# Kernel tuning notes

Measured on AMD Instinct MI355X. Metric: run time of the kernel, lower is better.

## Reference

```python
import jax, jax.numpy as jnp
import numpy as np

N, D, T = 4096, 512, 4096
TEMPERATURE = 0.07
MARGIN = 0.5
CONT_WEIGHT = 1.0
TRIP_WEIGHT = 0.3
EPS = 1e-8        # eps in the log / denominator (matches torch code)
PD_EPS = 1e-6     # F.pairwise_distance default eps added to the difference


def setup_inputs() -> dict:
    key = jax.random.key(0)
    k1, k2, k3 = jax.random.split(key, 3)
    embeddings = jax.random.normal(k1, (N, D), dtype=jnp.float32)
    labels = jax.random.randint(k2, (N,), 0, 256)            # ~16 positives per place
    triplets = jax.random.randint(k3, (T, 3), 0, N)          # (anchor, pos, neg) indices
    return {"embeddings": embeddings, "labels": labels, "triplets": triplets}


def reference(embeddings, labels, triplets):
    # ---- MultiPositiveContrastiveLoss ----
    # F.cosine_similarity normalizes each row with eps=1e-8 on the norm.
    norms = jnp.linalg.norm(embeddings, axis=1, keepdims=True)
    n_emb = embeddings / jnp.maximum(norms, EPS)
    sim = (n_emb @ n_emb.T) / TEMPERATURE                    # [N, N]

    pos_mask = (labels[:, None] == labels[None, :]).astype(embeddings.dtype)
    pos_mask = pos_mask * (1.0 - jnp.eye(sim.shape[0], dtype=embeddings.dtype))

    exp_sim = jnp.exp(sim)
    pos_sum = (exp_sim * pos_mask).sum(axis=1)
    total_sum = exp_sim.sum(axis=1)
    loss = -jnp.log(pos_sum / (total_sum + EPS) + EPS)

    valid = pos_mask.sum(axis=1) > 0
    cnt = valid.sum()
    cont_loss = jnp.where(
        cnt > 0,
        jnp.where(valid, loss, 0.0).sum() / jnp.maximum(cnt, 1).astype(loss.dtype),
        jnp.zeros((), loss.dtype),
    )

    # ---- TripletLoss, vectorized over all triplets (replaces Python loop) ----
    a = embeddings[triplets[:, 0]]   # [T, D]
    p = embeddings[triplets[:, 1]]
    ng = embeddings[triplets[:, 2]]
    pos_dist = jnp.linalg.norm(a - p + PD_EPS, axis=1)
    neg_dist = jnp.linalg.norm(a - ng + PD_EPS, axis=1)
    trip_loss = jnp.maximum(pos_dist - neg_dist + MARGIN, 0.0).mean()

    total = CONT_WEIGHT * cont_loss + TRIP_WEIGHT * trip_loss
    return (total, cont_loss, trip_loss)
```

## Files before the change

### kernel.cpp

```cpp
#include <hip/hip_runtime.h>

#define NN 4096
#define DD 512
#define TT 4096

typedef __bf16 bf16x8 __attribute__((ext_vector_type(8)));
typedef float f32x4 __attribute__((ext_vector_type(4)));

constexpr float INV_TEMP = 1.0f / 0.07f;

#define AS1(p) ((__attribute__((address_space(1))) const void*)(p))
#define AS3(p) ((__attribute__((address_space(3))) void*)(p))

__global__ __launch_bounds__(256) void k_normalize(const float* __restrict__ emb,
                                                   __bf16* __restrict__ nemb) {
    int wave = threadIdx.x >> 6, lane = threadIdx.x & 63;
    int row = blockIdx.x * 4 + wave;
    const float4* src = (const float4*)(emb + (size_t)row * DD);
    float4 x0 = src[lane * 2 + 0];
    float4 x1 = src[lane * 2 + 1];
    float ss = x0.x * x0.x + x0.y * x0.y + x0.z * x0.z + x0.w * x0.w +
               x1.x * x1.x + x1.y * x1.y + x1.z * x1.z + x1.w * x1.w;
    #pragma unroll
    for (int m = 1; m < 64; m <<= 1) ss += __shfl_xor(ss, m, 64);
    float inv = 1.0f / fmaxf(sqrtf(ss), 1e-8f);
    bf16x8 v;
    v[0] = (__bf16)(x0.x * inv); v[1] = (__bf16)(x0.y * inv);
    v[2] = (__bf16)(x0.z * inv); v[3] = (__bf16)(x0.w * inv);
    v[4] = (__bf16)(x1.x * inv); v[5] = (__bf16)(x1.y * inv);
    v[6] = (__bf16)(x1.z * inv); v[7] = (__bf16)(x1.w * inv);
    *(bf16x8*)(nemb + (size_t)row * DD + lane * 8) = v;
}

__global__ __launch_bounds__(256) void k_conttrip(const __bf16* __restrict__ nemb,
                                                  const int* __restrict__ labels,
                                                  const float* __restrict__ emb,
                                                  const int* __restrict__ trip,
                                                  float* __restrict__ posP,
                                                  float* __restrict__ totP,
                                                  float* __restrict__ cntP,
                                                  float* __restrict__ tl) {
    int tid = threadIdx.x;
    int lane = tid & 63, wave = tid >> 6;

    if (blockIdx.x >= 1024) {
        int t = (blockIdx.x - 1024) * 4 + wave;
        int ia = trip[t * 3 + 0], ip = trip[t * 3 + 1], ig = trip[t * 3 + 2];
        const float4* pa = (const float4*)(emb + (size_t)ia * DD);
        const float4* pp = (const float4*)(emb + (size_t)ip * DD);
        const float4* pn = (const float4*)(emb + (size_t)ig * DD);
        float d1 = 0.0f, d2 = 0.0f;
        #pragma unroll
        for (int j = 0; j < 2; ++j) {
            float4 a = pa[lane * 2 + j];
            float4 p = pp[lane * 2 + j];
            float4 n = pn[lane * 2 + j];
            float dx;
            dx = a.x - p.x + 1e-6f; d1 += dx * dx;
            dx = a.y - p.y + 1e-6f; d1 += dx * dx;
            dx = a.z - p.z + 1e-6f; d1 += dx * dx;
            dx = a.w - p.w + 1e-6f; d1 += dx * dx;
            dx = a.x - n.x + 1e-6f; d2 += dx * dx;
            dx = a.y - n.y + 1e-6f; d2 += dx * dx;
            dx = a.z - n.z + 1e-6f; d2 += dx * dx;
            dx = a.w - n.w + 1e-6f; d2 += dx * dx;
        }
        #pragma unroll
        for (int m = 1; m < 64; m <<= 1) {
            d1 += __shfl_xor(d1, m, 64);
            d2 += __shfl_xor(d2, m, 64);
        }
        if (lane == 0) tl[t] = fmaxf(sqrtf(d1) - sqrtf(d2) + 0.5f, 0.0f);
        return;
    }

    __shared__ __attribute__((aligned(16))) __bf16 aSm[128 * 64];
    __shared__ __attribute__((aligned(16))) __bf16 bSm[128 * 64];
    __shared__ int rlab[128];
    __shared__ int clab[128];

    int wr = wave >> 1, wc = wave & 1;
    int l15 = lane & 15, quad = lane >> 4;
    int rowblk = blockIdx.x >> 5, colblk = blockIdx.x & 31;
    int row0 = rowblk * 128, col0 = colblk * 128;

    if (tid < 128) rlab[tid] = labels[row0 + tid];
    else           clab[tid - 128] = labels[col0 + tid - 128];

    f32x4 acc[4][4];
    #pragma unroll
    for (int r = 0; r < 4; ++r)
        #pragma unroll
        for (int c = 0; c < 4; ++c) {
            f32x4 z = {0.0f, 0.0f, 0.0f, 0.0f};
            acc[r][c] = z;
        }

    const __bf16* gA = nemb + (size_t)(row0 + (tid >> 3)) * DD + (tid & 7) * 8;
    const __bf16* gB = nemb + (size_t)(col0 + (tid >> 3)) * DD + (tid & 7) * 8;

    for (int kt = 0; kt < 8; ++kt) {
        int kb = kt * 64;
        __syncthreads();
        #pragma unroll
        for (int op = 0; op < 4; ++op) {
            __builtin_amdgcn_global_load_lds(AS1(gA + (size_t)(32 * op) * DD + kb),
                                             AS3(aSm + op * 2048 + tid * 8), 16, 0, 0);
            __builtin_amdgcn_global_load_lds(AS1(gB + (size_t)(32 * op) * DD + kb),
                                             AS3(bSm + op * 2048 + tid * 8), 16, 0, 0);
        }
        __syncthreads();

        #pragma unroll
        for (int kc = 0; kc < 2; ++kc) {
            bf16x8 af[4], bfr[4];
            #pragma unroll
            for (int r = 0; r < 4; ++r)
                af[r] = *(const bf16x8*)(aSm + (wr * 64 + r * 16 + l15) * 64 + kc * 32 + quad * 8);
            #pragma unroll
            for (int c = 0; c < 4; ++c)
                bfr[c] = *(const bf16x8*)(bSm + (wc * 64 + c * 16 + l15) * 64 + kc * 32 + quad * 8);
            #pragma unroll
            for (int r = 0; r < 4; ++r)
                #pragma unroll
                for (int c = 0; c < 4; ++c)
                    acc[r][c] = __builtin_amdgcn_mfma_f32_16x16x32_bf16(af[r], bfr[c], acc[r][c], 0, 0, 0);
        }
    }

    int cl[4];
    #pragma unroll
    for (int c = 0; c < 4; ++c) cl[c] = clab[wc * 64 + c * 16 + l15];

    #pragma unroll
    for (int r = 0; r < 4; ++r) {
        float tv[4] = {0, 0, 0, 0}, pv[4] = {0, 0, 0, 0}, cv[4] = {0, 0, 0, 0};
        int gibase = row0 + wr * 64 + r * 16 + quad * 4;
        int rl[4];
        #pragma unroll
        for (int v = 0; v < 4; ++v) rl[v] = rlab[wr * 64 + r * 16 + quad * 4 + v];
        #pragma unroll
        for (int c = 0; c < 4; ++c) {
            int gj = col0 + wc * 64 + c * 16 + l15;
            #pragma unroll
            for (int v = 0; v < 4; ++v) {
                float e = __expf(acc[r][c][v] * INV_TEMP);
                tv[v] += e;
                bool match = (rl[v] == cl[c]) && ((gibase + v) != gj);
                pv[v] += match ? e : 0.0f;
                cv[v] += match ? 1.0f : 0.0f;
            }
        }
        #pragma unroll
        for (int m = 1; m < 16; m <<= 1) {
            #pragma unroll
            for (int v = 0; v < 4; ++v) {
                tv[v] += __shfl_xor(tv[v], m, 64);
                pv[v] += __shfl_xor(pv[v], m, 64);
                cv[v] += __shfl_xor(cv[v], m, 64);
            }
        }
        if (l15 == 0) {
            #pragma unroll
            for (int v = 0; v < 4; ++v) {
                int gr = gibase + v;
                int oidx = gr * 64 + colblk * 2 + wc;
                posP[oidx] = pv[v];
                totP[oidx] = tv[v];
                cntP[oidx] = cv[v];
            }
        }
    }
}

__global__ __launch_bounds__(256) void k_rowloss(const float* __restrict__ posP,
                                                 const float* __restrict__ totP,
                                                 const float* __restrict__ cntP,
                                                 float* __restrict__ rloss,
                                                 float* __restrict__ rvalid) {
    int wave = threadIdx.x >> 6, lane = threadIdx.x & 63;
    int row = blockIdx.x * 4 + wave;
    float p = posP[row * 64 + lane];
    float t = totP[row * 64 + lane];
    float c = cntP[row * 64 + lane];
    #pragma unroll
    for (int m = 1; m < 64; m <<= 1) {
        p += __shfl_xor(p, m, 64);
        t += __shfl_xor(t, m, 64);
        c += __shfl_xor(c, m, 64);
    }
    if (lane == 0) {
        float loss = -logf(p / (t + 1e-8f) + 1e-8f);
        bool valid = c > 0.0f;
        rloss[row] = valid ? loss : 0.0f;
        rvalid[row] = valid ? 1.0f : 0.0f;
    }
}

__global__ __launch_bounds__(256) void k_final(const float* __restrict__ rloss,
                                               const float* __restrict__ rvalid,
                                               const float* __restrict__ tl,
                                               float* __restrict__ out) {
    int tid = threadIdx.x;
    float sl = 0.0f, sv = 0.0f, st = 0.0f;
    for (int i = tid; i < NN; i += 256) {
        sl += rloss[i];
        sv += rvalid[i];
        st += tl[i];
    }
    #pragma unroll
    for (int m = 1; m < 64; m <<= 1) {
        sl += __shfl_xor(sl, m, 64);
        sv += __shfl_xor(sv, m, 64);
        st += __shfl_xor(st, m, 64);
    }
    __shared__ float red[3][4];
    int lane = tid & 63, wave = tid >> 6;
    if (lane == 0) { red[0][wave] = sl; red[1][wave] = sv; red[2][wave] = st; }
    __syncthreads();
    if (tid == 0) {
        float SL = red[0][0] + red[0][1] + red[0][2] + red[0][3];
        float SV = red[1][0] + red[1][1] + red[1][2] + red[1][3];
        float ST = red[2][0] + red[2][1] + red[2][2] + red[2][3];
        float cont = (SV > 0.0f) ? (SL / SV) : 0.0f;
        float trip = ST * (1.0f / (float)TT);
        out[0] = cont + 0.3f * trip;
        out[1] = cont;
        out[2] = trip;
    }
}

extern "C" void kernel_launch(void* const* d_in, const int* in_sizes, int n_in,
                              void* d_out, int out_size, void* d_ws, size_t ws_size,
                              hipStream_t stream) {
    const float* emb = (const float*)d_in[0];
    const int* labels = (const int*)d_in[1];
    const int* trips = (const int*)d_in[2];
    float* out = (float*)d_out;
    char* ws = (char*)d_ws;

    __bf16* nemb  = (__bf16*)(ws);
    float* posP   = (float*)(ws + 4194304);
    float* totP   = (float*)(ws + 5242880);
    float* cntP   = (float*)(ws + 6291456);
    float* rloss  = (float*)(ws + 7340032);
    float* rvalid = (float*)(ws + 7356416);
    float* tl     = (float*)(ws + 7372800);

    k_normalize<<<NN / 4, 256, 0, stream>>>(emb, nemb);
    k_conttrip<<<2048, 256, 0, stream>>>(nemb, labels, emb, trips, posP, totP, cntP, tl);
    k_rowloss<<<NN / 4, 256, 0, stream>>>(posP, totP, cntP, rloss, rvalid);
    k_final<<<1, 256, 0, stream>>>(rloss, rvalid, tl, out);
}
```

Baseline: 107.1 us.

## Rewrite contrastive GEMM as 256x256 double-buffered swizzled tile kernel; fuse triplet into normalize

The similarity GEMM now uses 256x256 output tiles per 512-thread block, with double-buffered LDS staging through global_load_lds, XOR-swizzled LDS layout, explicit vmcnt waits and phase-interleaved MFMA/load scheduling with setprio. The block-to-tile mapping is arranged per XCD for L2 locality. Triplet distance work moves from extra blocks in the GEMM kernel into the normalization kernel. This aims to raise MFMA utilization and hide load latency, at the cost of high register and LDS pressure and only 256 blocks, which may underfill the GPU.

```diff
diff --git a/kernel.cpp b/kernel.cpp
--- a/kernel.cpp
+++ b/kernel.cpp
@@ -12,10 +12,34 @@
 #define AS1(p) ((__attribute__((address_space(1))) const void*)(p))
 #define AS3(p) ((__attribute__((address_space(3))) void*)(p))
 
-__global__ __launch_bounds__(256) void k_normalize(const float* __restrict__ emb,
-                                                   __bf16* __restrict__ nemb) {
+__global__ __launch_bounds__(256) void k_normtrip(const float* __restrict__ emb,
+                                                  __bf16* __restrict__ nemb,
+                                                  const int* __restrict__ trip,
+                                                  float* __restrict__ tl) {
     int wave = threadIdx.x >> 6, lane = threadIdx.x & 63;
     int row = blockIdx.x * 4 + wave;
+
+    int ia = trip[row * 3 + 0], ip = trip[row * 3 + 1], ig = trip[row * 3 + 2];
+    const float4* pa = (const float4*)(emb + (size_t)ia * DD);
+    const float4* pp = (const float4*)(emb + (size_t)ip * DD);
+    const float4* pn = (const float4*)(emb + (size_t)ig * DD);
+    float d1 = 0.0f, d2 = 0.0f;
+    #pragma unroll
+    for (int j = 0; j < 2; ++j) {
+        float4 a = pa[lane * 2 + j];
+        float4 p = pp[lane * 2 + j];
+        float4 n = pn[lane * 2 + j];
+        float dx;
+        dx = a.x - p.x + 1e-6f; d1 += dx * dx;
+        dx = a.y - p.y + 1e-6f; d1 += dx * dx;
+        dx = a.z - p.z + 1e-6f; d1 += dx * dx;
+        dx = a.w - p.w + 1e-6f; d1 += dx * dx;
+        dx = a.x - n.x + 1e-6f; d2 += dx * dx;
+        dx = a.y - n.y + 1e-6f; d2 += dx * dx;
+        dx = a.z - n.z + 1e-6f; d2 += dx * dx;
+        dx = a.w - n.w + 1e-6f; d2 += dx * dx;
+    }
+
     const float4* src = (const float4*)(emb + (size_t)row * DD);
     float4 x0 = src[lane * 2 + 0];
     float4 x1 = src[lane * 2 + 1];
@@ -30,123 +54,171 @@
     v[4] = (__bf16)(x1.x * inv); v[5] = (__bf16)(x1.y * inv);
     v[6] = (__bf16)(x1.z * inv); v[7] = (__bf16)(x1.w * inv);
     *(bf16x8*)(nemb + (size_t)row * DD + lane * 8) = v;
-}
-
-__global__ __launch_bounds__(256) void k_conttrip(const __bf16* __restrict__ nemb,
-                                                  const int* __restrict__ labels,
-                                                  const float* __restrict__ emb,
-                                                  const int* __restrict__ trip,
-                                                  float* __restrict__ posP,
-                                                  float* __restrict__ totP,
-                                                  float* __restrict__ cntP,
-                                                  float* __restrict__ tl) {
+
+    #pragma unroll
+    for (int m = 1; m < 64; m <<= 1) {
+        d1 += __shfl_xor(d1, m, 64);
+        d2 += __shfl_xor(d2, m, 64);
+    }
+    if (lane == 0) tl[row] = fmaxf(sqrtf(d1) - sqrtf(d2) + 0.5f, 0.0f);
+}
+
+
+#define VMW(N) asm volatile("s_waitcnt vmcnt(" #N ")" ::: "memory")
+#define NOVM ((void)0)
+
+#define STAGE_A(T, H) do { \
+    const __bf16* g_ = nemb + (size_t)(row0 + (H) * 128 + srow) * DD + (T) * 64 + scol; \
+    __bf16* l_ = aSm + ((((T) & 1) * 2 + (H)) * 8192) + sdst; \
+    __builtin_amdgcn_global_load_lds(AS1(g_), AS3(l_), 16, 0, 0); \
+    __builtin_amdgcn_global_load_lds(AS1(g_ + (size_t)8 * DD), AS3(l_ + 512), 16, 0, 0); \
+} while (0)
+
+#define STAGE_B(T, H) do { \
+    const __bf16* g_ = nemb + (size_t)(col0 + (H) * 128 + srow) * DD + (T) * 64 + scol; \
+    __bf16* l_ = bSm + ((((T) & 1) * 2 + (H)) * 8192) + sdst; \
+    __builtin_amdgcn_global_load_lds(AS1(g_), AS3(l_), 16, 0, 0); \
+    __builtin_amdgcn_global_load_lds(AS1(g_ + (size_t)8 * DD), AS3(l_ + 512), 16, 0, 0); \
+} while (0)
+
+#define PHASE(LOADA, QM, QN, STAGE_STMT, VM_STMT) do { \
+    const __bf16* aB_ = aSm + (par * 2 + (QM)) * 8192; \
+    const __bf16* bB_ = bSm + (par * 2 + (QN)) * 8192; \
+    if (LOADA) { \
+        _Pragma("unroll") \
+        for (int fm_ = 0; fm_ < 4; ++fm_) { \
+            _Pragma("unroll") \
+            for (int kc_ = 0; kc_ < 2; ++kc_) \
+                af[fm_][kc_] = *(const bf16x8*)(aB_ + offA[fm_][kc_]); \
+        } \
+    } \
+    _Pragma("unroll") \
+    for (int fn_ = 0; fn_ < 2; ++fn_) { \
+        _Pragma("unroll") \
+        for (int kc_ = 0; kc_ < 2; ++kc_) \
+            bfr[fn_][kc_] = *(const bf16x8*)(bB_ + offB[fn_][kc_]); \
+    } \
+    STAGE_STMT; \
+    asm volatile("" ::: "memory"); \
+    __builtin_amdgcn_s_barrier(); \
+    asm volatile("s_waitcnt lgkmcnt(0)" ::: "memory"); \
+    __builtin_amdgcn_sched_barrier(0); \
+    __builtin_amdgcn_s_setprio(1); \
+    _Pragma("unroll") \
+    for (int kc_ = 0; kc_ < 2; ++kc_) { \
+        _Pragma("unroll") \
+        for (int fm_ = 0; fm_ < 4; ++fm_) { \
+            _Pragma("unroll") \
+            for (int fn_ = 0; fn_ < 2; ++fn_) \
+                acc[QM][QN][fm_][fn_] = __builtin_amdgcn_mfma_f32_16x16x32_bf16( \
+                    af[fm_][kc_], bfr[fn_][kc_], acc[QM][QN][fm_][fn_], 0, 0, 0); \
+        } \
+    } \
+    __builtin_amdgcn_s_setprio(0); \
+    __builtin_amdgcn_sched_barrier(0); \
+    VM_STMT; \
+    asm volatile("" ::: "memory"); \
+    __builtin_amdgcn_s_barrier(); \
+} while (0)
+
+#define GROUP(G, S12, S34, VM1, VM4) do { \
+    int par = (G) & 1; \
+    PHASE(1, 0, 0, { if (S12) STAGE_A((G) + 1, 1); }, VM1); \
+    PHASE(0, 0, 1, { if (S12) STAGE_B((G) + 1, 1); }, NOVM); \
+    PHASE(1, 1, 0, { if (S34) STAGE_A((G) + 2, 0); }, NOVM); \
+    PHASE(0, 1, 1, { if (S34) STAGE_B((G) + 2, 0); }, VM4); \
+} while (0)
+
+__global__ __launch_bounds__(512, 2) void k_contrast(const __bf16* __restrict__ nemb,
+                                                     const int* __restrict__ labels,
+                                                     float* __restrict__ posP,
+                                                     float* __restrict__ totP,
+                                                     float* __restrict__ cntP) {
+    __shared__ __attribute__((aligned(16))) __bf16 aSm[4 * 8192];
+    __shared__ __attribute__((aligned(16))) __bf16 bSm[4 * 8192];
+    __shared__ int rlab[256];
+    __shared__ int clab[256];
+
     int tid = threadIdx.x;
     int lane = tid & 63, wave = tid >> 6;
-
-    if (blockIdx.x >= 1024) {
-        int t = (blockIdx.x - 1024) * 4 + wave;
-        int ia = trip[t * 3 + 0], ip = trip[t * 3 + 1], ig = trip[t * 3 + 2];
-        const float4* pa = (const float4*)(emb + (size_t)ia * DD);
-        const float4* pp = (const float4*)(emb + (size_t)ip * DD);
-        const float4* pn = (const float4*)(emb + (size_t)ig * DD);
-        float d1 = 0.0f, d2 = 0.0f;
-        #pragma unroll
-        for (int j = 0; j < 2; ++j) {
-            float4 a = pa[lane * 2 + j];
-            float4 p = pp[lane * 2 + j];
-            float4 n = pn[lane * 2 + j];
-            float dx;
-            dx = a.x - p.x + 1e-6f; d1 += dx * dx;
-            dx = a.y - p.y + 1e-6f; d1 += dx * dx;
-            dx = a.z - p.z + 1e-6f; d1 += dx * dx;
-            dx = a.w - p.w + 1e-6f; d1 += dx * dx;
-            dx = a.x - n.x + 1e-6f; d2 += dx * dx;
-            dx = a.y - n.y + 1e-6f; d2 += dx * dx;
-            dx = a.z - n.z + 1e-6f; d2 += dx * dx;
-            dx = a.w - n.w + 1e-6f; d2 += dx * dx;
-        }
-        #pragma unroll
-        for (int m = 1; m < 64; m <<= 1) {
-            d1 += __shfl_xor(d1, m, 64);
-            d2 += __shfl_xor(d2, m, 64);
-        }
-        if (lane == 0) tl[t] = fmaxf(sqrtf(d1) - sqrtf(d2) + 0.5f, 0.0f);
-        return;
-    }
-
-    __shared__ __attribute__((aligned(16))) __bf16 aSm[128 * 64];
-    __shared__ __attribute__((aligned(16))) __bf16 bSm[128 * 64];
-    __shared__ int rlab[128];
-    __shared__ int clab[128];
-
-    int wr = wave >> 1, wc = wave & 1;
+    int wr = wave >> 2, wc = wave & 3;
     int l15 = lane & 15, quad = lane >> 4;
-    int rowblk = blockIdx.x >> 5, colblk = blockIdx.x & 31;
-    int row0 = rowblk * 128, col0 = colblk * 128;
-
-    if (tid < 128) rlab[tid] = labels[row0 + tid];
-    else           clab[tid - 128] = labels[col0 + tid - 128];
-
-    f32x4 acc[4][4];
-    #pragma unroll
-    for (int r = 0; r < 4; ++r)
-        #pragma unroll
-        for (int c = 0; c < 4; ++c) {
-            f32x4 z = {0.0f, 0.0f, 0.0f, 0.0f};
-            acc[r][c] = z;
-        }
-
-    const __bf16* gA = nemb + (size_t)(row0 + (tid >> 3)) * DD + (tid & 7) * 8;
-    const __bf16* gB = nemb + (size_t)(col0 + (tid >> 3)) * DD + (tid & 7) * 8;
-
-    for (int kt = 0; kt < 8; ++kt) {
-        int kb = kt * 64;
-        __syncthreads();
-        #pragma unroll
-        for (int op = 0; op < 4; ++op) {
-            __builtin_amdgcn_global_load_lds(AS1(gA + (size_t)(32 * op) * DD + kb),
-                                             AS3(aSm + op * 2048 + tid * 8), 16, 0, 0);
-            __builtin_amdgcn_global_load_lds(AS1(gB + (size_t)(32 * op) * DD + kb),
-                                             AS3(bSm + op * 2048 + tid * 8), 16, 0, 0);
-        }
-        __syncthreads();
-
-        #pragma unroll
-        for (int kc = 0; kc < 2; ++kc) {
-            bf16x8 af[4], bfr[4];
-            #pragma unroll
-            for (int r = 0; r < 4; ++r)
-                af[r] = *(const bf16x8*)(aSm + (wr * 64 + r * 16 + l15) * 64 + kc * 32 + quad * 8);
+    int swz = l15 & 7;
+
+    int bid = blockIdx.x;
+    int xcd = bid & 7, idx = bid >> 3;
+    int rowblk = (xcd >> 1) * 4 + (idx >> 3);
+    int colblk = (xcd & 1) * 8 + (idx & 7);
+    int row0 = rowblk * 256, col0 = colblk * 256;
+
+    if (tid < 256) rlab[tid] = labels[row0 + tid];
+    else           clab[tid - 256] = labels[col0 + tid - 256];
+
+    int srow = wave * 16 + ((tid >> 3) & 7);
+    int scol = ((tid & 7) ^ ((tid >> 3) & 7)) * 8;
+    int sdst = wave * 1024 + (tid & 63) * 8;
+
+    int offA[4][2], offB[2][2];
+    #pragma unroll
+    for (int fm = 0; fm < 4; ++fm)
+        #pragma unroll
+        for (int kc = 0; kc < 2; ++kc)
+            offA[fm][kc] = (wr * 64 + fm * 16 + l15) * 64 + (((kc * 4 + quad) ^ swz) * 8);
+    #pragma unroll
+    for (int fn = 0; fn < 2; ++fn)
+        #pragma unroll
+        for (int kc = 0; kc < 2; ++kc)
+            offB[fn][kc] = (wc * 32 + fn * 16 + l15) * 64 + (((kc * 4 + quad) ^ swz) * 8);
+
+    f32x4 acc[2][2][4][2];
+    #pragma unroll
+    for (int a = 0; a < 2; ++a)
+        #pragma unroll
+        for (int b = 0; b < 2; ++b)
             #pragma unroll
             for (int c = 0; c < 4; ++c)
-                bfr[c] = *(const bf16x8*)(bSm + (wc * 64 + c * 16 + l15) * 64 + kc * 32 + quad * 8);
-            #pragma unroll
-            for (int r = 0; r < 4; ++r)
                 #pragma unroll
-                for (int c = 0; c < 4; ++c)
-                    acc[r][c] = __builtin_amdgcn_mfma_f32_16x16x32_bf16(af[r], bfr[c], acc[r][c], 0, 0, 0);
-        }
-    }
-
-    int cl[4];
-    #pragma unroll
-    for (int c = 0; c < 4; ++c) cl[c] = clab[wc * 64 + c * 16 + l15];
-
-    #pragma unroll
-    for (int r = 0; r < 4; ++r) {
+                for (int d = 0; d < 2; ++d) {
+                    f32x4 z = {0.0f, 0.0f, 0.0f, 0.0f};
+                    acc[a][b][c][d] = z;
+                }
+
+    bf16x8 af[4][2], bfr[2][2];
+
+    STAGE_A(0, 0); STAGE_B(0, 0);
+    STAGE_A(0, 1); STAGE_B(0, 1);
+    STAGE_A(1, 0); STAGE_B(1, 0);
+    VMW(8);
+    asm volatile("" ::: "memory");
+    __builtin_amdgcn_s_barrier();
+
+    for (int g = 0; g < 6; ++g) GROUP(g, 1, 1, VMW(6), VMW(8));
+    GROUP(6, 1, 0, VMW(6), VMW(4));
+    GROUP(7, 0, 0, VMW(0), NOVM);
+
+    #pragma unroll
+    for (int qm = 0; qm < 2; ++qm)
+    #pragma unroll
+    for (int fm = 0; fm < 4; ++fm) {
+        int rloc = qm * 128 + wr * 64 + fm * 16 + quad * 4;
+        int gibase = row0 + rloc;
+        int rl[4];
+        #pragma unroll
+        for (int v = 0; v < 4; ++v) rl[v] = rlab[rloc + v];
         float tv[4] = {0, 0, 0, 0}, pv[4] = {0, 0, 0, 0}, cv[4] = {0, 0, 0, 0};
-        int gibase = row0 + wr * 64 + r * 16 + quad * 4;
-        int rl[4];
-        #pragma unroll
-        for (int v = 0; v < 4; ++v) rl[v] = rlab[wr * 64 + r * 16 + quad * 4 + v];
-        #pragma unroll
-        for (int c = 0; c < 4; ++c) {
-            int gj = col0 + wc * 64 + c * 16 + l15;
+        #pragma unroll
+        for (int qn = 0; qn < 2; ++qn)
+        #pragma unroll
+        for (int fn = 0; fn < 2; ++fn) {
+            int cloc = qn * 128 + wc * 32 + fn * 16 + l15;
+            int cl = clab[cloc];
+            int gj = col0 + cloc;
+            f32x4 a = acc[qm][qn][fm][fn];
             #pragma unroll
             for (int v = 0; v < 4; ++v) {
-                float e = __expf(acc[r][c][v] * INV_TEMP);
+                float e = __expf(a[v] * INV_TEMP);
                 tv[v] += e;
-                bool match = (rl[v] == cl[c]) && ((gibase + v) != gj);
+                bool match = (rl[v] == cl) && ((gibase + v) != gj);
                 pv[v] += match ? e : 0.0f;
                 cv[v] += match ? 1.0f : 0.0f;
             }
@@ -163,11 +235,10 @@
         if (l15 == 0) {
             #pragma unroll
             for (int v = 0; v < 4; ++v) {
-                int gr = gibase + v;
-                int oidx = gr * 64 + colblk * 2 + wc;
-                posP[oidx] = pv[v];
-                totP[oidx] = tv[v];
-                cntP[oidx] = cv[v];
+                int o = (gibase + v) * 64 + colblk * 4 + wc;
+                posP[o] = pv[v];
+                totP[o] = tv[v];
+                cntP[o] = cv[v];
             }
         }
     }
@@ -247,8 +318,8 @@
     float* rvalid = (float*)(ws + 7356416);
     float* tl     = (float*)(ws + 7372800);
 
-    k_normalize<<<NN / 4, 256, 0, stream>>>(emb, nemb);
-    k_conttrip<<<2048, 256, 0, stream>>>(nemb, labels, emb, trips, posP, totP, cntP, tl);
+    k_normtrip<<<NN / 4, 256, 0, stream>>>(emb, nemb, trips, tl);
+    k_contrast<<<256, 512, 0, stream>>>(nemb, labels, posP, totP, cntP);
     k_rowloss<<<NN / 4, 256, 0, stream>>>(posP, totP, cntP, rloss, rvalid);
     k_final<<<1, 256, 0, stream>>>(rloss, rvalid, tl, out);
 }
```

After: 101.5 us. 1.06x faster.
